# Performance work log

Measured on AMD Instinct MI355X. Metric: run time of the kernel, lower is better.

Reference implementation:

```python
import jax, jax.numpy as jnp
import numpy as np

LEAKY_SLOPE = 0.2
MASK_VAL = -9e15


def setup_inputs() -> dict:
    key = jax.random.key(0)
    k1, k2, k3, k4, k5, k6 = jax.random.split(key, 6)
    N_ex, N_kc, F_in, F_out = 20000, 1024, 128, 128
    exercise_h = jax.random.normal(k1, (N_ex, F_in), dtype=jnp.float32)
    kc_h = jax.random.normal(k2, (N_kc, F_in), dtype=jnp.float32)
    adj_exercise_kc = jax.random.randint(k3, (N_ex, N_kc), 0, 2, dtype=jnp.int32)
    # learned params (kaiming-ish scale)
    W1 = jax.random.normal(k4, (F_in, F_out), dtype=jnp.float32) * np.sqrt(2.0 / F_in)
    E = jax.random.normal(k5, (F_in, F_out), dtype=jnp.float32) * np.sqrt(2.0 / F_in)
    a = jax.random.normal(k6, (2 * F_out, 1), dtype=jnp.float32) * np.sqrt(2.0 / (2 * F_out))
    return {"exercise_h": exercise_h, "kc_h": kc_h,
            "adj_exercise_kc": adj_exercise_kc, "W1": W1, "E": E, "a": a}


def reference(exercise_h, kc_h, adj_exercise_kc, W1, E, a):
    F_out = W1.shape[1]
    kc_Wh = kc_h @ W1              # [N_kc, F_out]
    ex_Wh = exercise_h @ W1        # [N_ex, F_out]
    # Decompose a into halves: cat([ex_Wh_i, kc_Wh_j]) @ a == ex_Wh_i@a1 + kc_Wh_j@a2.
    a1, a2 = a[:F_out, 0], a[F_out:, 0]
    e = jax.nn.leaky_relu(ex_Wh @ a1[:, None] + (kc_Wh @ a2)[None, :],
                          negative_slope=LEAKY_SLOPE)   # [N_ex, N_kc]
    e = jnp.where(adj_exercise_kc > 0, e, MASK_VAL)
    attention = jax.nn.softmax(e, axis=1)
    new_kc_embed = attention @ kc_Wh               # [N_ex, F_out]
    exercise_Eh = exercise_h @ E                   # mode == 2
    return jax.nn.elu(new_kc_embed * exercise_Eh)
```

## Files before the change

### kernel.cpp

```cpp
#include <hip/hip_runtime.h>
#include <math.h>

#define N_EXC   20000
#define N_KCC   1024
#define FDIM    128
#define LEAKY_S 0.2f

#define BR  32
#define TJ  64
#define EXS 136
#define WST 72

typedef unsigned short ushort_t;
typedef __attribute__((ext_vector_type(8))) short short8;
typedef __attribute__((ext_vector_type(4))) float floatx4;

__device__ __forceinline__ ushort_t f2bf(float f) {
    unsigned u = __float_as_uint(f);
    u += 0x7FFF + ((u >> 16) & 1);
    return (ushort_t)(u >> 16);
}

__device__ __forceinline__ void async16(const void* g, void* l) {
    __builtin_amdgcn_global_load_lds(
        (const __attribute__((address_space(1))) unsigned int*)g,
        (__attribute__((address_space(3))) unsigned int*)l,
        16, 0, 0);
}


__global__ __launch_bounds__(256) void gat_prep(const float* __restrict__ kc_h,
                                                const float* __restrict__ W1,
                                                const float* __restrict__ E,
                                                const float* __restrict__ a,
                                                float* __restrict__ ws)
{
    float* tarr = ws;
    float* w1a1 = ws + N_KCC;
    ushort_t* kc_sw = (ushort_t*)(ws + N_KCC + FDIM);
    ushort_t* E_sw  = kc_sw + FDIM * N_KCC;
    const int tid = threadIdx.x;
    const int b = blockIdx.x;

    __shared__ __align__(16) float kct[128 * 132];
    __shared__ __align__(16) ushort_t sw[32 * 128];
    __shared__ __align__(16) float w1a2_lds[FDIM];

    if (b < 32) {
        const int jb = b >> 2, fq = b & 3;
        const float* kcbase = kc_h + (size_t)jb * 128 * FDIM;
        #pragma unroll
        for (int u = 0; u < 16; ++u) {
            int flat = u * 256 + tid;
            int r = flat >> 5, c4 = (flat & 31) * 4;
            float4 v = *(const float4*)(kcbase + r * FDIM + c4);
            kct[r * 132 + c4 + 0] = v.x; kct[r * 132 + c4 + 1] = v.y;
            kct[r * 132 + c4 + 2] = v.z; kct[r * 132 + c4 + 3] = v.w;
        }
        __syncthreads();
        const int jg = tid >> 4;
        const int fg = tid & 15;
        const int f0 = fq * 32 + fg * 2;
        float acc[8][2];
        #pragma unroll
        for (int i = 0; i < 8; ++i) { acc[i][0] = 0.f; acc[i][1] = 0.f; }
        for (int k4 = 0; k4 < FDIM; k4 += 4) {
            float4 av[8];
            #pragma unroll
            for (int i = 0; i < 8; ++i)
                av[i] = *(const float4*)(kct + (jg * 8 + i) * 132 + k4);
            #pragma unroll
            for (int kk = 0; kk < 4; ++kk) {
                float2 bv = *(const float2*)(W1 + (k4 + kk) * FDIM + f0);
                #pragma unroll
                for (int i = 0; i < 8; ++i) {
                    float a_ = ((const float*)&av[i])[kk];
                    acc[i][0] += a_ * bv.x;
                    acc[i][1] += a_ * bv.y;
                }
            }
        }
        #pragma unroll
        for (int c = 0; c < 2; ++c) {
            int f = f0 + c;
            int fl = fg * 2 + c;
            unsigned pk[4];
            #pragma unroll
            for (int i = 0; i < 4; ++i)
                pk[i] = (unsigned)f2bf(acc[2 * i][c]) | ((unsigned)f2bf(acc[2 * i + 1][c]) << 16);
            int jtl = jg >> 3;
            int cpp = (jg & 7) ^ (f & 7);
            *(uint4*)(sw + fl * 128 + jtl * 64 + cpp * 8) = make_uint4(pk[0], pk[1], pk[2], pk[3]);
        }
        __syncthreads();
        #pragma unroll
        for (int u = 0; u < 2; ++u) {
            int flat = u * 256 + tid;
            int fl = flat >> 4;
            int rem = flat & 15;
            int jtl = rem >> 3, cpp = rem & 7;
            ushort_t* dst = kc_sw + ((size_t)(jb * 2 + jtl)) * 8192
                          + (fq * 32 + fl) * 64 + cpp * 8;
            *(uint4*)dst = *(const uint4*)(sw + flat * 8);
        }
        return;
    }

    if (b < 36) {
        if (tid >= 128) {
            int k = tid - 128;
            float acc = 0.f;
            const float* row = W1 + k * FDIM;
            #pragma unroll 8
            for (int f = 0; f < FDIM; ++f) acc += row[f] * a[FDIM + f];
            w1a2_lds[k] = acc;
        } else if (b == 32) {
            float acc = 0.f;
            const float* row = W1 + tid * FDIM;
            #pragma unroll 8
            for (int f = 0; f < FDIM; ++f) acc += row[f] * a[f];
            w1a1[tid] = acc;
        }
        __syncthreads();
        int j = (b - 32) * 256 + tid;
        float s = 0.f;
        #pragma unroll 8
        for (int c = 0; c < 32; ++c) {
            float4 v = *(const float4*)(kc_h + (size_t)j * FDIM + c * 4);
            s += v.x * w1a2_lds[c * 4 + 0] + v.y * w1a2_lds[c * 4 + 1]
               + v.z * w1a2_lds[c * 4 + 2] + v.w * w1a2_lds[c * 4 + 3];
        }
        tarr[j] = s;
        return;
    }

    #pragma unroll
    for (int u = 0; u < 8; ++u) {
        int ch = u * 256 + tid;
        int half = ch >> 10;
        int rem = ch & 1023;
        int n = rem >> 3, cpp = rem & 7;
        int c = cpp ^ (n & 7);
        int kbase = half * 64 + c * 8;
        unsigned pk[4];
        #pragma unroll
        for (int i = 0; i < 4; ++i) {
            float e0 = E[(kbase + 2 * i + 0) * FDIM + n];
            float e1 = E[(kbase + 2 * i + 1) * FDIM + n];
            pk[i] = (unsigned)f2bf(e0) | ((unsigned)f2bf(e1) << 16);
        }
        *(uint4*)(E_sw + ch * 8) = make_uint4(pk[0], pk[1], pk[2], pk[3]);
    }
}

__global__ __launch_bounds__(256, 3) void gat_main(const float* __restrict__ ex_h,
                                                   const int* __restrict__ adj,
                                                   const float* __restrict__ ws,
                                                   float* __restrict__ out)
{
    const float* tarr = ws;
    const float* w1a1 = ws + N_KCC;
    const ushort_t* kc_sw = (const ushort_t*)(ws + N_KCC + FDIM);
    const ushort_t* E_sw  = kc_sw + FDIM * N_KCC;

    __shared__ __align__(16) float t_lds[N_KCC];
    __shared__ __align__(16) ushort_t kc_lds[2 * 8192];
    __shared__ __align__(16) ushort_t ww_lds[4608];
    __shared__ __align__(16) float scrA[256];
    __shared__ __align__(16) float scrB[256];
    __shared__ float w1a1_lds[FDIM];
    __shared__ float s_lds[BR], m_lds[BR], denom_lds[BR];

    const int tid  = threadIdx.x;
    const int R0   = blockIdx.x * BR;
    const int lane = tid & 63, wid = tid >> 6;
    const int l15  = lane & 15, quad = lane >> 4;

    #pragma unroll
    for (int u = 0; u < 8; ++u) {
        int ci = u * 256 + tid;
        async16(E_sw + ci * 8, kc_lds + ci * 8);
    }

    #pragma unroll
    for (int u = 0; u < 4; ++u) t_lds[u * 256 + tid] = tarr[u * 256 + tid];
    if (tid < FDIM) w1a1_lds[tid] = w1a1[tid];
    const int r0 = tid >> 3;
    const int fc = (tid & 7) * 16;
    float exv[16];
    {
        const float* src = ex_h + (size_t)(R0 + r0) * FDIM + fc;
        #pragma unroll
        for (int c = 0; c < 4; ++c) {
            float4 v = *(const float4*)(src + c * 4);
            exv[c * 4 + 0] = v.x; exv[c * 4 + 1] = v.y;
            exv[c * 4 + 2] = v.z; exv[c * 4 + 3] = v.w;
        }
        unsigned pk[8];
        #pragma unroll
        for (int i = 0; i < 8; ++i)
            pk[i] = (unsigned)f2bf(exv[2 * i]) | ((unsigned)f2bf(exv[2 * i + 1]) << 16);
        *(uint4*)(ww_lds + r0 * EXS + fc)     = make_uint4(pk[0], pk[1], pk[2], pk[3]);
        *(uint4*)(ww_lds + r0 * EXS + fc + 8) = make_uint4(pk[4], pk[5], pk[6], pk[7]);
    }

    const int r_w = tid >> 3;
    const int jg  = tid & 7;
    const int* abase = adj + (size_t)(R0 + r_w) * N_KCC + jg * 8;
    unsigned msk[4];
    #pragma unroll
    for (int g = 0; g < 4; ++g) {
        int4 q0 = *(const int4*)(abase + (g * 4 + 0) * 64);
        int4 q1 = *(const int4*)(abase + (g * 4 + 0) * 64 + 4);
        int4 q2 = *(const int4*)(abase + (g * 4 + 1) * 64);
        int4 q3 = *(const int4*)(abase + (g * 4 + 1) * 64 + 4);
        int4 q4 = *(const int4*)(abase + (g * 4 + 2) * 64);
        int4 q5 = *(const int4*)(abase + (g * 4 + 2) * 64 + 4);
        int4 q6 = *(const int4*)(abase + (g * 4 + 3) * 64);
        int4 q7 = *(const int4*)(abase + (g * 4 + 3) * 64 + 4);
        unsigned m = 0;
        m |= (q0.x > 0 ? 1u : 0u) << 0;  m |= (q0.y > 0 ? 1u : 0u) << 1;
        m |= (q0.z > 0 ? 1u : 0u) << 2;  m |= (q0.w > 0 ? 1u : 0u) << 3;
        m |= (q1.x > 0 ? 1u : 0u) << 4;  m |= (q1.y > 0 ? 1u : 0u) << 5;
        m |= (q1.z > 0 ? 1u : 0u) << 6;  m |= (q1.w > 0 ? 1u : 0u) << 7;
        m |= (q2.x > 0 ? 1u : 0u) << 8;  m |= (q2.y > 0 ? 1u : 0u) << 9;
        m |= (q2.z > 0 ? 1u : 0u) << 10; m |= (q2.w > 0 ? 1u : 0u) << 11;
        m |= (q3.x > 0 ? 1u : 0u) << 12; m |= (q3.y > 0 ? 1u : 0u) << 13;
        m |= (q3.z > 0 ? 1u : 0u) << 14; m |= (q3.w > 0 ? 1u : 0u) << 15;
        m |= (q4.x > 0 ? 1u : 0u) << 16; m |= (q4.y > 0 ? 1u : 0u) << 17;
        m |= (q4.z > 0 ? 1u : 0u) << 18; m |= (q4.w > 0 ? 1u : 0u) << 19;
        m |= (q5.x > 0 ? 1u : 0u) << 20; m |= (q5.y > 0 ? 1u : 0u) << 21;
        m |= (q5.z > 0 ? 1u : 0u) << 22; m |= (q5.w > 0 ? 1u : 0u) << 23;
        m |= (q6.x > 0 ? 1u : 0u) << 24; m |= (q6.y > 0 ? 1u : 0u) << 25;
        m |= (q6.z > 0 ? 1u : 0u) << 26; m |= (q6.w > 0 ? 1u : 0u) << 27;
        m |= (q7.x > 0 ? 1u : 0u) << 28; m |= (q7.y > 0 ? 1u : 0u) << 29;
        m |= (q7.z > 0 ? 1u : 0u) << 30; m |= (q7.w > 0 ? 1u : 0u) << 31;
        msk[g] = m;
    }
    __syncthreads();

    {
        float mx = fmaxf(fmaxf(t_lds[tid], t_lds[256 + tid]),
                         fmaxf(t_lds[512 + tid], t_lds[768 + tid]));
        scrB[tid] = mx;
        float p = 0.f;
        #pragma unroll
        for (int i = 0; i < 16; ++i) p += exv[i] * w1a1_lds[fc + i];
        scrA[tid] = p;
    }
    __syncthreads();
    if (tid < 64)
        scrB[tid] = fmaxf(fmaxf(scrB[tid], scrB[tid + 64]),
                          fmaxf(scrB[tid + 128], scrB[tid + 192]));
    __syncthreads();
    if (tid < BR) {
        float Tm = scrB[0];
        #pragma unroll 8
        for (int i = 1; i < 64; ++i) Tm = fmaxf(Tm, scrB[i]);
        float s = 0.f;
        #pragma unroll
        for (int g = 0; g < 8; ++g) s += scrA[tid * 8 + g];
        s_lds[tid] = s;
        float x = s + Tm;
        m_lds[tid] = (x >= 0.f) ? x : LEAKY_S * x;
    }
    __syncthreads();

    floatx4 eh_acc[2][2], att_acc[2][2];
    #pragma unroll
    for (int mg = 0; mg < 2; ++mg)
        #pragma unroll
        for (int h = 0; h < 2; ++h) {
            eh_acc[mg][h]  = (floatx4){0.f, 0.f, 0.f, 0.f};
            att_acc[mg][h] = (floatx4){0.f, 0.f, 0.f, 0.f};
        }
    #pragma unroll
    for (int kk = 0; kk < 4; ++kk) {
        short8 a0 = *(const short8*)(ww_lds + l15 * EXS + kk * 32 + quad * 8);
        short8 a1 = *(const short8*)(ww_lds + (16 + l15) * EXS + kk * 32 + quad * 8);
        #pragma unroll
        for (int h = 0; h < 2; ++h) {
            const int n = (h * 4 + wid) * 16 + l15;
            const int cpp = ((kk & 1) * 4 + quad) ^ (n & 7);
            short8 bf = *(const short8*)(kc_lds + (kk >> 1) * 8192 + n * 64 + cpp * 8);
            eh_acc[0][h] = __builtin_amdgcn_mfma_f32_16x16x32_bf16(a0, bf, eh_acc[0][h], 0, 0, 0);
            eh_acc[1][h] = __builtin_amdgcn_mfma_f32_16x16x32_bf16(a1, bf, eh_acc[1][h], 0, 0, 0);
        }
    }
    __syncthreads();

    const float sr = s_lds[r_w];
    const float mr = m_lds[r_w];
    float denom_part = 0.f;

    auto genw = [&](int jt, ushort_t* wb) {
        const int jb = jt * TJ + jg * 8;
        float4 ta = *(const float4*)(t_lds + jb);
        float4 tb = *(const float4*)(t_lds + jb + 4);
        float tv[8] = {ta.x, ta.y, ta.z, ta.w, tb.x, tb.y, tb.z, tb.w};
        unsigned mb = msk[jt >> 2] >> ((jt & 3) * 8);
        float wv[8];
        #pragma unroll
        for (int e = 0; e < 8; ++e) {
            float x = sr + tv[e];
            x = fmaxf(x, LEAKY_S * x);
            float w = __expf(x - mr);
            w = ((mb >> e) & 1u) ? w : 0.f;
            denom_part += w;
            wv[e] = w;
        }
        unsigned pk[4];
        #pragma unroll
        for (int i = 0; i < 4; ++i) {
            unsigned ua = __float_as_uint(wv[2 * i + 0]) + 0x8000u;
            unsigned ub = __float_as_uint(wv[2 * i + 1]) + 0x8000u;
            pk[i] = __builtin_amdgcn_perm(ub, ua, 0x07060302);
        }
        *(uint4*)(wb + r_w * WST + jg * 8) = make_uint4(pk[0], pk[1], pk[2], pk[3]);
    };

    #pragma unroll
    for (int u = 0; u < 4; ++u) {
        int ci = u * 256 + tid;
        async16(kc_sw + ci * 8, kc_lds + ci * 8);
    }
    genw(0, ww_lds);
    __syncthreads();

    for (int jt = 0; jt < N_KCC / TJ; ++jt) {
        if (jt < 15) {
            const ushort_t* gsrc = kc_sw + (size_t)(jt + 1) * 8192;
            ushort_t* kdst = kc_lds + ((jt + 1) & 1) * 8192;
            #pragma unroll
            for (int u = 0; u < 4; ++u) {
                int ci = u * 256 + tid;
                async16(gsrc + ci * 8, kdst + ci * 8);
            }
            genw(jt + 1, ww_lds + ((jt + 1) & 1) * 2304);
        }
        const ushort_t* kcb = kc_lds + (jt & 1) * 8192;
        const ushort_t* wb  = ww_lds + (jt & 1) * 2304;
        #pragma unroll
        for (int kk = 0; kk < 2; ++kk) {
            short8 a0 = *(const short8*)(wb + l15 * WST + kk * 32 + quad * 8);
            short8 a1 = *(const short8*)(wb + (16 + l15) * WST + kk * 32 + quad * 8);
            #pragma unroll
            for (int h = 0; h < 2; ++h) {
                const int f = (h * 4 + wid) * 16 + l15;
                const int cpp = (kk * 4 + quad) ^ (f & 7);
                short8 bf = *(const short8*)(kcb + f * 64 + cpp * 8);
                att_acc[0][h] = __builtin_amdgcn_mfma_f32_16x16x32_bf16(a0, bf, att_acc[0][h], 0, 0, 0);
                att_acc[1][h] = __builtin_amdgcn_mfma_f32_16x16x32_bf16(a1, bf, att_acc[1][h], 0, 0, 0);
            }
        }
        __syncthreads();
    }

    scrA[tid] = denom_part;
    __syncthreads();
    if (tid < BR) {
        float d = 0.f;
        #pragma unroll
        for (int g = 0; g < 8; ++g) d += scrA[tid * 8 + g];
        denom_lds[tid] = (d > 0.f) ? d : 1.f;
    }
    __syncthreads();

    #pragma unroll
    for (int mg = 0; mg < 2; ++mg) {
        float rd[4];
        #pragma unroll
        for (int reg = 0; reg < 4; ++reg)
            rd[reg] = 1.f / denom_lds[mg * 16 + quad * 4 + reg];
        #pragma unroll
        for (int h = 0; h < 2; ++h) {
            const int col = (h * 4 + wid) * 16 + l15;
            #pragma unroll
            for (int reg = 0; reg < 4; ++reg) {
                const int rl = mg * 16 + quad * 4 + reg;
                float v = att_acc[mg][h][reg] * rd[reg] * eh_acc[mg][h][reg];
                out[(size_t)(R0 + rl) * FDIM + col] = (v > 0.f) ? v : expm1f(v);
            }
        }
    }
}

extern "C" void kernel_launch(void* const* d_in, const int* in_sizes, int n_in,
                              void* d_out, int out_size, void* d_ws, size_t ws_size,
                              hipStream_t stream)
{
    const float* ex_h = (const float*)d_in[0];
    const float* kc_h = (const float*)d_in[1];
    const int*   adj  = (const int*)d_in[2];
    const float* W1   = (const float*)d_in[3];
    const float* E    = (const float*)d_in[4];
    const float* a    = (const float*)d_in[5];
    float* outp = (float*)d_out;
    float* ws   = (float*)d_ws;

    gat_prep<<<37, 256, 0, stream>>>(kc_h, W1, E, a, ws);
    gat_main<<<N_EXC / BR, 256, 0, stream>>>(ex_h, adj, ws, outp);
}
```

Baseline: 164.7 us.

## Split prep into two kernels and compute kc_h@W1 with bf16 MFMA

The single prep kernel is split in two. The first builds a transposed, swizzled bf16 copy of W1 plus w1a1 and the E layout. The second uses 64 blocks running MFMA 16x16x32 bf16 to compute kc_h@W1, and derives the tarr scores from the same accumulators rather than a separate dot product. This replaces the scalar FP32 GEMM in prep and spreads the work over more blocks, at the cost of an extra kernel launch and bf16 rounding of kc_h before the multiply. Since the change touches only prep, while gat_main over 20000 rows likely dominates, any gain is bounded.

```diff
diff --git a/kernel.cpp b/kernel.cpp
--- a/kernel.cpp
+++ b/kernel.cpp
@@ -29,127 +29,153 @@
 }
 
 
-__global__ __launch_bounds__(256) void gat_prep(const float* __restrict__ kc_h,
-                                                const float* __restrict__ W1,
-                                                const float* __restrict__ E,
-                                                const float* __restrict__ a,
-                                                float* __restrict__ ws)
+__global__ __launch_bounds__(256) void gat_prep0(const float* __restrict__ W1,
+                                                 const float* __restrict__ E,
+                                                 const float* __restrict__ a,
+                                                 float* __restrict__ ws)
+{
+    float* w1a1 = ws + N_KCC;
+    ushort_t* kc_sw  = (ushort_t*)(ws + N_KCC + FDIM);
+    ushort_t* E_sw   = kc_sw + FDIM * N_KCC;
+    ushort_t* W1T_sw = E_sw + FDIM * FDIM;
+    const int tid = threadIdx.x;
+
+    if (blockIdx.x == 1) {
+        #pragma unroll
+        for (int u = 0; u < 8; ++u) {
+            int ch = u * 256 + tid;
+            int half = ch >> 10;
+            int rem = ch & 1023;
+            int n = rem >> 3, cpp = rem & 7;
+            int c = cpp ^ (n & 7);
+            int kbase = half * 64 + c * 8;
+            unsigned pk[4];
+            #pragma unroll
+            for (int i = 0; i < 4; ++i) {
+                float e0 = E[(kbase + 2 * i + 0) * FDIM + n];
+                float e1 = E[(kbase + 2 * i + 1) * FDIM + n];
+                pk[i] = (unsigned)f2bf(e0) | ((unsigned)f2bf(e1) << 16);
+            }
+            *(uint4*)(E_sw + ch * 8) = make_uint4(pk[0], pk[1], pk[2], pk[3]);
+        }
+        return;
+    }
+
+    __shared__ __align__(16) float w1f[128 * 132];
+    __shared__ float a_lds[2 * FDIM];
+    #pragma unroll
+    for (int u = 0; u < 16; ++u) {
+        int flat = u * 256 + tid;
+        int k = flat >> 5, c4 = (flat & 31) * 4;
+        float4 v = *(const float4*)(W1 + k * FDIM + c4);
+        w1f[k * 132 + c4 + 0] = v.x; w1f[k * 132 + c4 + 1] = v.y;
+        w1f[k * 132 + c4 + 2] = v.z; w1f[k * 132 + c4 + 3] = v.w;
+    }
+    a_lds[tid] = a[tid];
+    __syncthreads();
+    #pragma unroll
+    for (int u = 0; u < 8; ++u) {
+        int ch = u * 256 + tid;
+        int f = ch >> 4, c = ch & 15;
+        unsigned pk[4];
+        #pragma unroll
+        for (int i = 0; i < 4; ++i) {
+            float v0 = w1f[(c * 8 + 2 * i + 0) * 132 + f];
+            float v1 = w1f[(c * 8 + 2 * i + 1) * 132 + f];
+            pk[i] = (unsigned)f2bf(v0) | ((unsigned)f2bf(v1) << 16);
+        }
+        *(uint4*)(W1T_sw + f * 128 + (c ^ (f & 15)) * 8) = make_uint4(pk[0], pk[1], pk[2], pk[3]);
+    }
+    if (tid < FDIM) {
+        float acc = 0.f;
+        #pragma unroll 8
+        for (int f = 0; f < FDIM; ++f) acc += w1f[tid * 132 + f] * a_lds[f];
+        w1a1[tid] = acc;
+    }
+}
+
+__global__ __launch_bounds__(256) void gat_prep1(const float* __restrict__ kc_h,
+                                                 const float* __restrict__ a,
+                                                 float* __restrict__ ws)
 {
     float* tarr = ws;
-    float* w1a1 = ws + N_KCC;
-    ushort_t* kc_sw = (ushort_t*)(ws + N_KCC + FDIM);
-    ushort_t* E_sw  = kc_sw + FDIM * N_KCC;
+    ushort_t* kc_sw  = (ushort_t*)(ws + N_KCC + FDIM);
+    ushort_t* E_sw   = kc_sw + FDIM * N_KCC;
+    const ushort_t* W1T_sw = E_sw + FDIM * FDIM;
+
+    __shared__ __align__(16) ushort_t w1t[128 * 128];
+    __shared__ __align__(16) ushort_t outt[128 * 16];
+    __shared__ float a2_lds[FDIM];
+    __shared__ float scrT[256];
+
     const int tid = threadIdx.x;
     const int b = blockIdx.x;
-
-    __shared__ __align__(16) float kct[128 * 132];
-    __shared__ __align__(16) ushort_t sw[32 * 128];
-    __shared__ __align__(16) float w1a2_lds[FDIM];
-
-    if (b < 32) {
-        const int jb = b >> 2, fq = b & 3;
-        const float* kcbase = kc_h + (size_t)jb * 128 * FDIM;
-        #pragma unroll
-        for (int u = 0; u < 16; ++u) {
-            int flat = u * 256 + tid;
-            int r = flat >> 5, c4 = (flat & 31) * 4;
-            float4 v = *(const float4*)(kcbase + r * FDIM + c4);
-            kct[r * 132 + c4 + 0] = v.x; kct[r * 132 + c4 + 1] = v.y;
-            kct[r * 132 + c4 + 2] = v.z; kct[r * 132 + c4 + 3] = v.w;
-        }
-        __syncthreads();
-        const int jg = tid >> 4;
-        const int fg = tid & 15;
-        const int f0 = fq * 32 + fg * 2;
-        float acc[8][2];
-        #pragma unroll
-        for (int i = 0; i < 8; ++i) { acc[i][0] = 0.f; acc[i][1] = 0.f; }
-        for (int k4 = 0; k4 < FDIM; k4 += 4) {
-            float4 av[8];
-            #pragma unroll
-            for (int i = 0; i < 8; ++i)
-                av[i] = *(const float4*)(kct + (jg * 8 + i) * 132 + k4);
-            #pragma unroll
-            for (int kk = 0; kk < 4; ++kk) {
-                float2 bv = *(const float2*)(W1 + (k4 + kk) * FDIM + f0);
-                #pragma unroll
-                for (int i = 0; i < 8; ++i) {
-                    float a_ = ((const float*)&av[i])[kk];
-                    acc[i][0] += a_ * bv.x;
-                    acc[i][1] += a_ * bv.y;
-                }
-            }
-        }
-        #pragma unroll
-        for (int c = 0; c < 2; ++c) {
-            int f = f0 + c;
-            int fl = fg * 2 + c;
-            unsigned pk[4];
-            #pragma unroll
-            for (int i = 0; i < 4; ++i)
-                pk[i] = (unsigned)f2bf(acc[2 * i][c]) | ((unsigned)f2bf(acc[2 * i + 1][c]) << 16);
-            int jtl = jg >> 3;
-            int cpp = (jg & 7) ^ (f & 7);
-            *(uint4*)(sw + fl * 128 + jtl * 64 + cpp * 8) = make_uint4(pk[0], pk[1], pk[2], pk[3]);
-        }
-        __syncthreads();
-        #pragma unroll
-        for (int u = 0; u < 2; ++u) {
-            int flat = u * 256 + tid;
-            int fl = flat >> 4;
-            int rem = flat & 15;
-            int jtl = rem >> 3, cpp = rem & 7;
-            ushort_t* dst = kc_sw + ((size_t)(jb * 2 + jtl)) * 8192
-                          + (fq * 32 + fl) * 64 + cpp * 8;
-            *(uint4*)dst = *(const uint4*)(sw + flat * 8);
-        }
-        return;
-    }
-
-    if (b < 36) {
-        if (tid >= 128) {
-            int k = tid - 128;
-            float acc = 0.f;
-            const float* row = W1 + k * FDIM;
-            #pragma unroll 8
-            for (int f = 0; f < FDIM; ++f) acc += row[f] * a[FDIM + f];
-            w1a2_lds[k] = acc;
-        } else if (b == 32) {
-            float acc = 0.f;
-            const float* row = W1 + tid * FDIM;
-            #pragma unroll 8
-            for (int f = 0; f < FDIM; ++f) acc += row[f] * a[f];
-            w1a1[tid] = acc;
-        }
-        __syncthreads();
-        int j = (b - 32) * 256 + tid;
+    const int j0 = b * 16;
+    const int jt = b >> 2;
+    const int c0 = (b & 3) * 2;
+    const int lane = tid & 63, w = tid >> 6;
+    const int l15 = lane & 15, quad = lane >> 4;
+
+    #pragma unroll
+    for (int u = 0; u < 8; ++u) {
+        int ci = u * 256 + tid;
+        async16(W1T_sw + ci * 8, w1t + ci * 8);
+    }
+    if (tid < FDIM) a2_lds[tid] = a[FDIM + tid];
+
+    short8 bfrag[4];
+    #pragma unroll
+    for (int kk = 0; kk < 4; ++kk) {
+        const float* p = kc_h + (size_t)(j0 + l15) * FDIM + kk * 32 + quad * 8;
+        float4 x = *(const float4*)(p);
+        float4 y = *(const float4*)(p + 4);
+        float v[8] = {x.x, x.y, x.z, x.w, y.x, y.y, y.z, y.w};
+        unsigned pk[4];
+        #pragma unroll
+        for (int i = 0; i < 4; ++i)
+            pk[i] = (unsigned)f2bf(v[2 * i]) | ((unsigned)f2bf(v[2 * i + 1]) << 16);
+        uint4 q = make_uint4(pk[0], pk[1], pk[2], pk[3]);
+        bfrag[kk] = *(const short8*)&q;
+    }
+    __syncthreads();
+
+    floatx4 acc[2];
+    acc[0] = (floatx4){0.f, 0.f, 0.f, 0.f};
+    acc[1] = (floatx4){0.f, 0.f, 0.f, 0.f};
+    #pragma unroll
+    for (int kk = 0; kk < 4; ++kk) {
+        #pragma unroll
+        for (int g = 0; g < 2; ++g) {
+            int f = w * 32 + g * 16 + l15;
+            int cp = (kk * 4 + quad) ^ l15;
+            short8 af = *(const short8*)(w1t + f * 128 + cp * 8);
+            acc[g] = __builtin_amdgcn_mfma_f32_16x16x32_bf16(af, bfrag[kk], acc[g], 0, 0, 0);
+        }
+    }
+
+    float tp = 0.f;
+    #pragma unroll
+    for (int g = 0; g < 2; ++g)
+        #pragma unroll
+        for (int reg = 0; reg < 4; ++reg) {
+            int f = w * 32 + g * 16 + quad * 4 + reg;
+            outt[f * 16 + l15] = f2bf(acc[g][reg]);
+            tp += acc[g][reg] * a2_lds[f];
+        }
+    scrT[l15 * 16 + w * 4 + quad] = tp;
+    __syncthreads();
+
+    {
+        int f = tid >> 1, hf = tid & 1;
+        uint4 v = *(const uint4*)(outt + f * 16 + hf * 8);
+        int cp = (c0 + hf) ^ (f & 7);
+        *(uint4*)(kc_sw + (size_t)jt * 8192 + f * 64 + cp * 8) = v;
+    }
+    if (tid < 16) {
         float s = 0.f;
-        #pragma unroll 8
-        for (int c = 0; c < 32; ++c) {
-            float4 v = *(const float4*)(kc_h + (size_t)j * FDIM + c * 4);
-            s += v.x * w1a2_lds[c * 4 + 0] + v.y * w1a2_lds[c * 4 + 1]
-               + v.z * w1a2_lds[c * 4 + 2] + v.w * w1a2_lds[c * 4 + 3];
-        }
-        tarr[j] = s;
-        return;
-    }
-
-    #pragma unroll
-    for (int u = 0; u < 8; ++u) {
-        int ch = u * 256 + tid;
-        int half = ch >> 10;
-        int rem = ch & 1023;
-        int n = rem >> 3, cpp = rem & 7;
-        int c = cpp ^ (n & 7);
-        int kbase = half * 64 + c * 8;
-        unsigned pk[4];
-        #pragma unroll
-        for (int i = 0; i < 4; ++i) {
-            float e0 = E[(kbase + 2 * i + 0) * FDIM + n];
-            float e1 = E[(kbase + 2 * i + 1) * FDIM + n];
-            pk[i] = (unsigned)f2bf(e0) | ((unsigned)f2bf(e1) << 16);
-        }
-        *(uint4*)(E_sw + ch * 8) = make_uint4(pk[0], pk[1], pk[2], pk[3]);
+        #pragma unroll
+        for (int p = 0; p < 16; ++p) s += scrT[tid * 16 + p];
+        tarr[j0 + tid] = s;
     }
 }
 
@@ -398,6 +424,7 @@
     float* outp = (float*)d_out;
     float* ws   = (float*)d_ws;
 
-    gat_prep<<<37, 256, 0, stream>>>(kc_h, W1, E, a, ws);
+    gat_prep0<<<2, 256, 0, stream>>>(W1, E, a, ws);
+    gat_prep1<<<64, 256, 0, stream>>>(kc_h, a, ws);
     gat_main<<<N_EXC / BR, 256, 0, stream>>>(ex_h, adj, ws, outp);
 }
```

Result: slower. 168.4 us (+2.2%).
